# Performance work log

Measured on AMD Instinct MI355X. Metric: run time of the kernel, lower is better.

Reference implementation:

```python
import jax, jax.numpy as jnp
import numpy as np

EPS = 1e-5

def lrelu(x):
    return jnp.where(x > 0, x, 0.2 * x)

def bn(x, g, b, ch_axis=1):
    # BatchNorm in training-mode math (batch statistics), affine
    axes = tuple(i for i in range(x.ndim) if i != ch_axis)
    m = x.mean(axes, keepdims=True)
    v = x.var(axes, keepdims=True)
    shp = [1] * x.ndim; shp[ch_axis] = -1
    return g.reshape(shp) * (x - m) / jnp.sqrt(v + EPS) + b.reshape(shp)

def get_graph_feature(x, idx):
    # x: (B,C,N), idx: (B,N,k) -> edge features (B,2C,N,k) = [neighbor - center, center]
    xt = jnp.transpose(x, (0, 2, 1))                      # (B,N,C)
    nb = jax.vmap(lambda pts, i: pts[i])(xt, idx)         # gather: (B,N,k,C)
    center = jnp.broadcast_to(xt[:, :, None, :], nb.shape)
    edge = jnp.concatenate([nb - center, center], axis=-1)  # (B,N,k,2C)
    return jnp.transpose(edge, (0, 3, 1, 2))              # (B,2C,N,k)

def setup_inputs() -> dict:
    key = jax.random.key(0)
    ks = jax.random.split(key, 12)
    B, N, K = 4, 2048, 20
    def w(k, o, c, s=0.05):
        return jax.random.normal(k, (o, c), jnp.float32) * s
    inp = {}
    inp["x"] = jax.random.normal(ks[0], (B, N, 3), jnp.float32)
    inp["start_neighs"] = jax.random.randint(ks[1], (B, N, K), 0, N)
    dims = [(6, 64), (128, 128), (256, 256), (512, 512)]
    for i, (ci, co) in enumerate(dims):
        inp["w%d" % i] = w(ks[2 + i], co, ci)
        inp["g%d" % i] = jnp.ones((co,), jnp.float32)
        inp["b%d" % i] = jnp.zeros((co,), jnp.float32)
    inp["w4"] = w(ks[6], 1024, 960)
    inp["g4"] = jnp.ones((1024,), jnp.float32); inp["b4"] = jnp.zeros((1024,), jnp.float32)
    inp["lw1"] = w(ks[7], 1024, 2048)
    inp["g6"] = jnp.ones((1024,), jnp.float32); inp["b6"] = jnp.zeros((1024,), jnp.float32)
    inp["lw2"] = w(ks[8], 512, 1024); inp["lb2"] = jnp.zeros((512,), jnp.float32)
    inp["g7"] = jnp.ones((512,), jnp.float32); inp["b7"] = jnp.zeros((512,), jnp.float32)
    inp["lw3"] = w(ks[9], 256, 512); inp["lb3"] = jnp.zeros((256,), jnp.float32)
    return inp

def reference(x, start_neighs,
              w0, g0, b0, w1, g1, b1, w2, g2, b2, w3, g3, b3,
              w4, g4, b4, lw1, g6, b6, lw2, lb2, g7, b7, lw3, lb3):
    # forward_per_point
    xt = jnp.transpose(x, (0, 2, 1))                      # (B,3,N)
    h = get_graph_feature(xt, start_neighs)               # (B,6,N,k)
    outs = []
    for (w, g, b) in ((w0, g0, b0), (w1, g1, b1), (w2, g2, b2), (w3, g3, b3)):
        if outs:  # only_true_neighs=True -> reuse start_neighs
            h = get_graph_feature(outs[-1], start_neighs)
        h = lrelu(bn(jnp.einsum('oc,bcnk->bonk', w, h), g, b))  # 1x1 Conv2d + BN + LeakyReLU
        outs.append(h.max(axis=-1))                       # max over k neighbors -> (B,C,N)
    cat = jnp.concatenate(outs, axis=1)                   # (B,960,N)
    feats = lrelu(bn(jnp.einsum('oc,bcn->bon', w4, cat), g4, b4))  # (B,1024,N)
    # aggregate_all_points (dropout p=0 -> identity)
    z = jnp.concatenate([feats.max(-1), feats.mean(-1)], axis=1)   # (B,2048)
    z = lrelu(bn(z @ lw1.T, g6, b6))
    z = lrelu(bn(z @ lw2.T + lb2, g7, b7))
    z = z @ lw3.T + lb3                                   # (B,256)
    # forward returns (aggregated.squeeze(-1), features_per_point.transpose(1,2)) = (z, (B,1024,N))
    return z, feats
```

## Files before the change

kernel.cpp:

```cpp
#include <hip/hip_runtime.h>
#include <cstddef>
#include <cstdint>

#define EPSBN 1e-5f
constexpr int B_ = 4, N_ = 2048, K_ = 20;

typedef __attribute__((ext_vector_type(8))) _Float16 half8v;
typedef __attribute__((ext_vector_type(4))) float f32x4;
typedef const __attribute__((address_space(1))) unsigned int* gas_t;
typedef __attribute__((address_space(3))) unsigned int* las_t;

__device__ __forceinline__ void swz_batch(int B, int& b, int& local) {
    b = (B & 7) >> 1;
    local = ((B >> 3) << 1) | (B & 1);
}


__device__ __forceinline__ void prep_conv(const float* __restrict__ W, _Float16* __restrict__ W2h,
                                          int O, int C, int i) {
    int o = i / C, c = i - o * C;
    float a = W[o * 2 * C + c];
    float d = W[o * 2 * C + C + c] - a;
    W2h[(size_t)o * C + c] = (_Float16)a;
    W2h[(size_t)(O + o) * C + c] = (_Float16)d;
}

__global__ void k_prep_all(const float* __restrict__ w1, const float* __restrict__ w2,
                           const float* __restrict__ w3, const float* __restrict__ w4,
                           _Float16* __restrict__ W2h1, _Float16* __restrict__ W2h2,
                           _Float16* __restrict__ W2h3, _Float16* __restrict__ w4h) {
    int i = blockIdx.x * 256 + threadIdx.x;
    if (i < 8192) { prep_conv(w1, W2h1, 128, 64, i); return; }
    i -= 8192;
    if (i < 32768) { prep_conv(w2, W2h2, 256, 128, i); return; }
    i -= 32768;
    if (i < 131072) { prep_conv(w3, W2h3, 512, 256, i); return; }
    i -= 131072;
    if (i < 983040) w4h[i] = (_Float16)w4[i];
}

__global__ void k_dense0(const float* __restrict__ x, const float* __restrict__ w0,
                         _Float16* __restrict__ Z0) {
    int b, local;
    swz_batch(blockIdx.x, b, local);
    int i = (b * 1024 + local) * 256 + threadIdx.x;
    int p = i >> 7, o = i & 127;
    float x0 = x[p * 3], x1 = x[p * 3 + 1], x2 = x[p * 3 + 2];
    float r;
    if (o < 64) {
        r = x0 * w0[o * 6] + x1 * w0[o * 6 + 1] + x2 * w0[o * 6 + 2];
    } else {
        int oo = o - 64;
        r = x0 * (w0[oo * 6 + 3] - w0[oo * 6]) + x1 * (w0[oo * 6 + 4] - w0[oo * 6 + 1]) +
            x2 * (w0[oo * 6 + 5] - w0[oo * 6 + 2]);
    }
    Z0[i] = (_Float16)r;
}

template<bool STATS>
__global__ __launch_bounds__(256, 3)
void k_gemm(const _Float16* __restrict__ A, int sa,
            const _Float16* __restrict__ Bw, int K,
            _Float16* __restrict__ outp, int so,
            float* __restrict__ psum, float* __restrict__ psq) {
    __shared__ __align__(16) _Float16 Als[128 * 64];
    __shared__ __align__(16) _Float16 Bls[128 * 64];
    const int tid = threadIdx.x, lane = tid & 63, w = tid >> 6;
    int bsw, lsw;
    swz_batch(blockIdx.x, bsw, lsw);
    const int m0 = (bsw * 16 + lsw) * 128;
    const int n0 = blockIdx.y * 128;
    const int wr = (w >> 1) * 64, wc = (w & 1) * 64;

    f32x4 acc[4][4];
#pragma unroll
    for (int i = 0; i < 4; ++i)
#pragma unroll
        for (int j = 0; j < 4; ++j) acc[i][j] = (f32x4){0.f, 0.f, 0.f, 0.f};

    int srow[4], scol[4];
#pragma unroll
    for (int j = 0; j < 4; ++j) {
        int idx = w * 256 + j * 64 + lane;
        srow[j] = idx >> 3;
        scol[j] = ((idx & 7) ^ (srow[j] & 7)) * 8;
    }
    int aoff[4][2], boff[4][2];
#pragma unroll
    for (int i = 0; i < 4; ++i) {
        int ra = wr + i * 16 + (lane & 15);
        int rb = wc + i * 16 + (lane & 15);
#pragma unroll
        for (int t = 0; t < 2; ++t) {
            aoff[i][t] = ra * 64 + ((((lane >> 4) + t * 4) ^ (ra & 7)) * 8);
            boff[i][t] = rb * 64 + ((((lane >> 4) + t * 4) ^ (rb & 7)) * 8);
        }
    }

    for (int c0 = 0; c0 < K; c0 += 64) {
#pragma unroll
        for (int j = 0; j < 4; ++j) {
            const _Float16* ga = &A[(size_t)(m0 + srow[j]) * sa + c0 + scol[j]];
            const _Float16* gb = &Bw[(size_t)(n0 + srow[j]) * K + c0 + scol[j]];
            __builtin_amdgcn_global_load_lds((gas_t)(const void*)ga,
                                             (las_t)(void*)&Als[(w * 256 + j * 64) * 8], 16, 0, 0);
            __builtin_amdgcn_global_load_lds((gas_t)(const void*)gb,
                                             (las_t)(void*)&Bls[(w * 256 + j * 64) * 8], 16, 0, 0);
        }
        __syncthreads();
#pragma unroll
        for (int t = 0; t < 2; ++t) {
            half8v a[4], b[4];
#pragma unroll
            for (int i = 0; i < 4; ++i) {
                a[i] = *(const half8v*)&Als[aoff[i][t]];
                b[i] = *(const half8v*)&Bls[boff[i][t]];
            }
#pragma unroll
            for (int i = 0; i < 4; ++i)
#pragma unroll
                for (int j = 0; j < 4; ++j)
                    acc[i][j] = __builtin_amdgcn_mfma_f32_16x16x32_f16(a[i], b[j], acc[i][j], 0, 0, 0);
        }
        __syncthreads();
    }
#pragma unroll
    for (int i = 0; i < 4; ++i)
#pragma unroll
        for (int j = 0; j < 4; ++j)
#pragma unroll
            for (int e = 0; e < 4; ++e) {
                int row = m0 + wr + i * 16 + (lane >> 4) * 4 + e;
                int col = n0 + wc + j * 16 + (lane & 15);
                outp[(size_t)row * so + col] = (_Float16)acc[i][j][e];
            }
    if constexpr (STATS) {
        int slice = blockIdx.x & 63;
#pragma unroll
        for (int j = 0; j < 4; ++j) {
            float s = 0.f, q = 0.f;
#pragma unroll
            for (int i = 0; i < 4; ++i)
#pragma unroll
                for (int e = 0; e < 4; ++e) {
                    float v = acc[i][j][e];
                    s += v; q += v * v;
                }
            s += __shfl_xor(s, 16); s += __shfl_xor(s, 32);
            q += __shfl_xor(q, 16); q += __shfl_xor(q, 32);
            if ((lane >> 4) == 0) {
                int col = n0 + wc + j * 16 + lane;
                atomicAdd(&psum[slice * 1024 + col], s);
                atomicAdd(&psq[slice * 1024 + col], q);
            }
        }
    }
}

template<int O>
__global__ __launch_bounds__(256)
void k_gather(const _Float16* __restrict__ Z, const int* __restrict__ nidx,
              const float* __restrict__ g,
              _Float16* __restrict__ exth,
              float* __restrict__ psum, float* __restrict__ psq) {
    constexpr int VPT = O / 8, P = 256 / VPT;
    __shared__ float s_red[P * O];
    __shared__ float q_red[P * O];
    const int tid = threadIdx.x;
    const int pl = tid / VPT, v = tid % VPT;
    int bsw, local;
    swz_batch(blockIdx.x, bsw, local);
    const int bbase = bsw * N_;
    const int p = bbase + local * P + pl;
    float sg[8];
#pragma unroll
    for (int e = 0; e < 8; ++e) sg[e] = (g[v * 8 + e] >= 0.f) ? 1.f : -1.f;
    float mx[8], sm[8], sq[8];
#pragma unroll
    for (int e = 0; e < 8; ++e) { mx[e] = -3.4e38f; sm[e] = 0.f; sq[e] = 0.f; }
    const int* np = nidx + p * K_;
#pragma unroll 4
    for (int k = 0; k < K_; ++k) {
        int j = np[k];
        half8v z = *(const half8v*)&Z[(size_t)(bbase + j) * (2 * O) + v * 8];
#pragma unroll
        for (int e = 0; e < 8; ++e) {
            float f = (float)z[e];
            mx[e] = fmaxf(mx[e], f * sg[e]);
            sm[e] += f;
            sq[e] += f * f;
        }
    }
    half8v zd = *(const half8v*)&Z[(size_t)p * (2 * O) + O + v * 8];
    const float Kf = (float)K_;
    half8v exo;
#pragma unroll
    for (int e = 0; e < 8; ++e) {
        float zf = (float)zd[e];
        exo[e] = (_Float16)(sg[e] * mx[e] + zf);
        s_red[pl * O + v * 8 + e] = sm[e] + Kf * zf;
        q_red[pl * O + v * 8 + e] = sq[e] + 2.f * zf * sm[e] + Kf * zf * zf;
    }
    *(half8v*)&exth[(size_t)p * O + v * 8] = exo;
    __syncthreads();
    int slice = blockIdx.x & 63;
    for (int ch = tid; ch < O; ch += 256) {
        float s = 0.f, q = 0.f;
#pragma unroll
        for (int pp = 0; pp < P; ++pp) { s += s_red[pp * O + ch]; q += q_red[pp * O + ch]; }
        atomicAdd(&psum[slice * 1024 + ch], s);
        atomicAdd(&psq[slice * 1024 + ch], q);
    }
}

__global__ void k_finalize_sl(const float* __restrict__ psum, const float* __restrict__ psq,
                              const float* __restrict__ g, const float* __restrict__ b,
                              float cntInv, int O,
                              float* __restrict__ scale, float* __restrict__ shift) {
    int o = blockIdx.x * 256 + threadIdx.x;
    if (o >= O) return;
    float s = 0.f, q = 0.f;
    for (int i = 0; i < 64; ++i) { s += psum[i * 1024 + o]; q += psq[i * 1024 + o]; }
    float m = s * cntInv;
    float v = q * cntInv - m * m;
    float sc = g[o] * rsqrtf(fmaxf(v, 0.f) + EPSBN);
    scale[o] = sc;
    shift[o] = b[o] - m * sc;
}

template<int O>
__global__ void k_bn_apply(const _Float16* __restrict__ exth,
                           const float* __restrict__ scale, const float* __restrict__ shift,
                           _Float16* __restrict__ cath, int coff) {
    constexpr int PPB = 2048 / O;
    int bsw, local;
    swz_batch(blockIdx.x, bsw, local);
    const int pt_base = bsw * N_ + local * PPB;
    int tid = threadIdx.x;
    int pt = pt_base + (tid * 8) / O;
    int v8 = (tid * 8) & (O - 1);
    half8v hx = *(const half8v*)&exth[(size_t)pt * O + v8];
    half8v r;
#pragma unroll
    for (int e = 0; e < 8; ++e) {
        int o = v8 + e;
        float y = scale[o] * (float)hx[e] + shift[o];
        y = y > 0.f ? y : 0.2f * y;
        r[e] = (_Float16)y;
    }
    *(half8v*)&cath[(size_t)pt * 960 + coff + v8] = r;
}

__global__ void k_feats_out(const _Float16* __restrict__ Y4, const float* __restrict__ scale,
                            const float* __restrict__ shift, float* __restrict__ fo,
                            float* __restrict__ pmax, float* __restrict__ psumn) {
    __shared__ float tile[32][33];
    int tx = threadIdx.x, ty = threadIdx.y;
    int b = blockIdx.z;
    int n0 = blockIdx.x * 32, c0 = blockIdx.y * 32;
#pragma unroll
    for (int i = 0; i < 4; ++i) {
        int n = n0 + ty + i * 8;
        int c = c0 + tx;
        float v = (float)Y4[((size_t)(b * N_ + n)) * 1024 + c];
        v = scale[c] * v + shift[c];
        v = v > 0.f ? v : 0.2f * v;
        tile[ty + i * 8][tx] = v;
    }
    __syncthreads();
#pragma unroll
    for (int i = 0; i < 4; ++i) {
        int c = c0 + ty + i * 8;
        int n = n0 + tx;
        float v2 = tile[tx][ty + i * 8];
        fo[((size_t)(b * 1024 + c)) * N_ + n] = v2;
        float mx = v2, s = v2;
#pragma unroll
        for (int d = 1; d < 32; d <<= 1) {
            mx = fmaxf(mx, __shfl_xor(mx, d));
            s += __shfl_xor(s, d);
        }
        if (tx == 0) {
            int bc = (b << 10) + c;
            pmax[(size_t)bc * 64 + blockIdx.x] = mx;
            psumn[(size_t)bc * 64 + blockIdx.x] = s;
        }
    }
}

__global__ void k_pool2(const float* __restrict__ pmax, const float* __restrict__ psumn,
                        float* __restrict__ z0) {
    int bc = blockIdx.x * 4 + (threadIdx.x >> 6);
    int lane = threadIdx.x & 63;
    float mx = pmax[(size_t)bc * 64 + lane];
    float s  = psumn[(size_t)bc * 64 + lane];
#pragma unroll
    for (int d = 1; d < 64; d <<= 1) {
        mx = fmaxf(mx, __shfl_xor(mx, d));
        s += __shfl_xor(s, d);
    }
    if (lane == 0) {
        int b = bc >> 10, c = bc & 1023;
        z0[b * 2048 + c] = mx;
        z0[b * 2048 + 1024 + c] = s * (1.f / N_);
    }
}

__global__ void k_fc(const float* __restrict__ zin, const float* __restrict__ W,
                     const float* __restrict__ bias,
                     const float* __restrict__ gg, const float* __restrict__ gb,
                     int C, int O, float* __restrict__ zout) {
    __shared__ float sh4[4];
    const int b = threadIdx.x >> 6;
    const int lane = threadIdx.x & 63;
    const int o = blockIdx.x;
    const float* wr = W + (size_t)o * C;
    const float* zr = zin + b * C;
    float s = 0.f;
    for (int c = lane * 4; c < C; c += 256) {
        const float4 wv = *(const float4*)&wr[c];
        const float4 zv = *(const float4*)&zr[c];
        s += wv.x * zv.x + wv.y * zv.y + wv.z * zv.z + wv.w * zv.w;
    }
    s += __shfl_xor(s, 1);
    s += __shfl_xor(s, 2);
    s += __shfl_xor(s, 4);
    s += __shfl_xor(s, 8);
    s += __shfl_xor(s, 16);
    s += __shfl_xor(s, 32);
    if (!gg) {
        if (lane == 0) zout[b * O + o] = s + (bias ? bias[o] : 0.f);
        return;
    }
    if (lane == 0) sh4[b] = s + (bias ? bias[o] : 0.f);
    __syncthreads();
    if (threadIdx.x == 0) {
        float v0 = sh4[0], v1 = sh4[1], v2 = sh4[2], v3 = sh4[3];
        float m = 0.25f * (v0 + v1 + v2 + v3);
        float d0 = v0 - m, d1 = v1 - m, d2 = v2 - m, d3 = v3 - m;
        float var = 0.25f * (d0 * d0 + d1 * d1 + d2 * d2 + d3 * d3);
        float sc = gg[o] * rsqrtf(var + EPSBN);
        float shv = gb[o];
        float r0 = sc * d0 + shv, r1 = sc * d1 + shv, r2 = sc * d2 + shv, r3 = sc * d3 + shv;
        zout[o]         = r0 > 0.f ? r0 : 0.2f * r0;
        zout[O + o]     = r1 > 0.f ? r1 : 0.2f * r1;
        zout[2 * O + o] = r2 > 0.f ? r2 : 0.2f * r2;
        zout[3 * O + o] = r3 > 0.f ? r3 : 0.2f * r3;
    }
}


extern "C" void kernel_launch(void* const* d_in, const int* in_sizes, int n_in,
                              void* d_out, int out_size, void* d_ws, size_t ws_size,
                              hipStream_t stream) {
    const float* x    = (const float*)d_in[0];
    const int*   nidx = (const int*)d_in[1];
    const float* w[5]  = {(const float*)d_in[2], (const float*)d_in[5], (const float*)d_in[8],
                          (const float*)d_in[11], (const float*)d_in[14]};
    const float* g[5]  = {(const float*)d_in[3], (const float*)d_in[6], (const float*)d_in[9],
                          (const float*)d_in[12], (const float*)d_in[15]};
    const float* bb[5] = {(const float*)d_in[4], (const float*)d_in[7], (const float*)d_in[10],
                          (const float*)d_in[13], (const float*)d_in[16]};
    const float* lw1 = (const float*)d_in[17];
    const float* g6  = (const float*)d_in[18];
    const float* b6  = (const float*)d_in[19];
    const float* lw2 = (const float*)d_in[20];
    const float* lb2 = (const float*)d_in[21];
    const float* g7  = (const float*)d_in[22];
    const float* b7  = (const float*)d_in[23];
    const float* lw3 = (const float*)d_in[24];
    const float* lb3 = (const float*)d_in[25];

    float* out = (float*)d_out;
    float* fo  = out + 1024;

    uint8_t* base8 = (uint8_t*)d_ws;
    size_t off = 0;
    auto alloc = [&](size_t bytes) -> void* {
        void* r = base8 + off;
        off += (bytes + 255) & ~(size_t)255;
        return r;
    };
    _Float16* cath = (_Float16*)alloc((size_t)B_ * N_ * 960 * 2);
    _Float16* Z    = (_Float16*)alloc((size_t)8192 * 1024 * 2);
    _Float16* exth = (_Float16*)alloc((size_t)8192 * 512 * 2);
    _Float16* Y4   = (_Float16*)alloc((size_t)8192 * 1024 * 2);
    _Float16* W2h1 = (_Float16*)alloc((size_t)256 * 64 * 2);
    _Float16* W2h2 = (_Float16*)alloc((size_t)512 * 128 * 2);
    _Float16* W2h3 = (_Float16*)alloc((size_t)1024 * 256 * 2);
    _Float16* w4h  = (_Float16*)alloc((size_t)1024 * 960 * 2);
    float* psumall = (float*)alloc((size_t)5 * 131072 * 4);
    float* pmax  = (float*)alloc((size_t)4096 * 64 * 4);
    float* psumn = (float*)alloc((size_t)4096 * 64 * 4);
    float* scalev= (float*)alloc(1024 * 4);
    float* shiftv= (float*)alloc(1024 * 4);
    float* z0    = (float*)alloc(8192 * 4);
    float* z1    = (float*)alloc(4096 * 4);
    float* z2    = (float*)alloc(2048 * 4);
    (void)ws_size; (void)in_sizes; (void)n_in; (void)out_size;

    auto psumR = [&](int r) { return psumall + (size_t)r * 131072; };
    auto psqR  = [&](int r) { return psumall + (size_t)r * 131072 + 65536; };

    hipMemsetAsync(psumall, 0, (size_t)5 * 131072 * 4, stream);
    k_prep_all<<<(8192 + 32768 + 131072 + 983040 + 255) / 256, 256, 0, stream>>>(
        w[1], w[2], w[3], w[4], W2h1, W2h2, W2h3, w4h);

    k_dense0<<<4096, 256, 0, stream>>>(x, w[0], Z);
    k_gather<64><<<256, 256, 0, stream>>>(Z, nidx, g[0], exth, psumR(0), psqR(0));
    k_finalize_sl<<<1, 256, 0, stream>>>(psumR(0), psqR(0), g[0], bb[0], 1.f / (B_ * N_ * K_),
                                         64, scalev, shiftv);
    k_bn_apply<64><<<256, 256, 0, stream>>>(exth, scalev, shiftv, cath, 0);

    struct LayerCfg { int coff_in, C, O, coff_out, li; const _Float16* Wh; };
    const LayerCfg L[3] = {
        { 0,   64,  128, 64,  1, W2h1 },
        { 64,  128, 256, 192, 2, W2h2 },
        { 192, 256, 512, 448, 3, W2h3 },
    };
    for (int i = 0; i < 3; ++i) {
        const LayerCfg& Lc = L[i];
        dim3 ggrid(64, (2 * Lc.O) / 128);
        k_gemm<false><<<ggrid, 256, 0, stream>>>(cath + Lc.coff_in, 960, Lc.Wh, Lc.C,
                                                 Z, 2 * Lc.O, nullptr, nullptr);
        if (Lc.O == 128) {
            k_gather<128><<<512, 256, 0, stream>>>(Z, nidx, g[Lc.li], exth, psumR(i + 1), psqR(i + 1));
            k_finalize_sl<<<1, 256, 0, stream>>>(psumR(i + 1), psqR(i + 1), g[Lc.li], bb[Lc.li],
                                                 1.f / (B_ * N_ * K_), 128, scalev, shiftv);
            k_bn_apply<128><<<512, 256, 0, stream>>>(exth, scalev, shiftv, cath, Lc.coff_out);
        } else if (Lc.O == 256) {
            k_gather<256><<<1024, 256, 0, stream>>>(Z, nidx, g[Lc.li], exth, psumR(i + 1), psqR(i + 1));
            k_finalize_sl<<<1, 256, 0, stream>>>(psumR(i + 1), psqR(i + 1), g[Lc.li], bb[Lc.li],
                                                 1.f / (B_ * N_ * K_), 256, scalev, shiftv);
            k_bn_apply<256><<<1024, 256, 0, stream>>>(exth, scalev, shiftv, cath, Lc.coff_out);
        } else {
            k_gather<512><<<2048, 256, 0, stream>>>(Z, nidx, g[Lc.li], exth, psumR(i + 1), psqR(i + 1));
            k_finalize_sl<<<2, 256, 0, stream>>>(psumR(i + 1), psqR(i + 1), g[Lc.li], bb[Lc.li],
                                                 1.f / (B_ * N_ * K_), 512, scalev, shiftv);
            k_bn_apply<512><<<2048, 256, 0, stream>>>(exth, scalev, shiftv, cath, Lc.coff_out);
        }
    }

    k_gemm<true><<<dim3(64, 8), 256, 0, stream>>>(cath, 960, w4h, 960, Y4, 1024, psumR(4), psqR(4));
    k_finalize_sl<<<4, 256, 0, stream>>>(psumR(4), psqR(4), g[4], bb[4], 1.f / (B_ * N_), 1024,
                                         scalev, shiftv);
    k_feats_out<<<dim3(64, 32, 4), dim3(32, 8), 0, stream>>>(Y4, scalev, shiftv, fo, pmax, psumn);
    k_pool2<<<1024, 256, 0, stream>>>(pmax, psumn, z0);

    k_fc<<<1024, 256, 0, stream>>>(z0, lw1, nullptr, g6, b6, 2048, 1024, z1);
    k_fc<<<512, 256, 0, stream>>>(z1, lw2, lb2, g7, b7, 1024, 512, z2);
    k_fc<<<256, 256, 0, stream>>>(z2, lw3, lb3, nullptr, nullptr, 512, 256, out);
}
```

Measured before the change: 172.0 us.

## Fuse BN stat finalization into producers via last-block counter; fuse layer-0 dense into gather

Removes the separate k_finalize_sl launches by having the last block of each stats-producing kernel (tracked with an atomic counter and threadfence) compute the BN scale and shift. It also folds the layer-0 pointwise conv into a new gather kernel that computes features directly from xyz coordinates, which drops k_dense0 and its Z round-trip. Together these remove five launches and one intermediate buffer write. The cost is a serialized tail in one block per kernel, plus extra atomic counter traffic.

Result: slower. 552.8 us (+221.3%).

```diff
diff --git a/kernel.cpp b/kernel.cpp
--- a/kernel.cpp
+++ b/kernel.cpp
@@ -13,6 +13,39 @@
 __device__ __forceinline__ void swz_batch(int B, int& b, int& local) {
     b = (B & 7) >> 1;
     local = ((B >> 3) << 1) | (B & 1);
+}
+
+__device__ __forceinline__ float agent_load(const float* p) {
+    return __hip_atomic_load(p, __ATOMIC_RELAXED, __HIP_MEMORY_SCOPE_AGENT);
+}
+
+__device__ __forceinline__ void finalize_tail(const float* __restrict__ psum,
+                                              const float* __restrict__ psq,
+                                              const float* __restrict__ g,
+                                              const float* __restrict__ b,
+                                              float cntInv, int O, int nblk,
+                                              float* __restrict__ scale,
+                                              float* __restrict__ shift,
+                                              int* __restrict__ cnt) {
+    __shared__ int s_last;
+    __threadfence();
+    __syncthreads();
+    if (threadIdx.x == 0) s_last = (atomicAdd(cnt, 1) == nblk - 1);
+    __syncthreads();
+    if (!s_last) return;
+    for (int o = threadIdx.x; o < O; o += 256) {
+        float s = 0.f, q = 0.f;
+#pragma unroll 8
+        for (int i = 0; i < 64; ++i) {
+            s += agent_load(&psum[i * 1024 + o]);
+            q += agent_load(&psq[i * 1024 + o]);
+        }
+        float m = s * cntInv;
+        float v = q * cntInv - m * m;
+        float sc = g[o] * rsqrtf(fmaxf(v, 0.f) + EPSBN);
+        scale[o] = sc;
+        shift[o] = b[o] - m * sc;
+    }
 }
 
 
@@ -39,30 +72,14 @@
     if (i < 983040) w4h[i] = (_Float16)w4[i];
 }
 
-__global__ void k_dense0(const float* __restrict__ x, const float* __restrict__ w0,
-                         _Float16* __restrict__ Z0) {
-    int b, local;
-    swz_batch(blockIdx.x, b, local);
-    int i = (b * 1024 + local) * 256 + threadIdx.x;
-    int p = i >> 7, o = i & 127;
-    float x0 = x[p * 3], x1 = x[p * 3 + 1], x2 = x[p * 3 + 2];
-    float r;
-    if (o < 64) {
-        r = x0 * w0[o * 6] + x1 * w0[o * 6 + 1] + x2 * w0[o * 6 + 2];
-    } else {
-        int oo = o - 64;
-        r = x0 * (w0[oo * 6 + 3] - w0[oo * 6]) + x1 * (w0[oo * 6 + 4] - w0[oo * 6 + 1]) +
-            x2 * (w0[oo * 6 + 5] - w0[oo * 6 + 2]);
-    }
-    Z0[i] = (_Float16)r;
-}
-
 template<bool STATS>
 __global__ __launch_bounds__(256, 3)
 void k_gemm(const _Float16* __restrict__ A, int sa,
             const _Float16* __restrict__ Bw, int K,
             _Float16* __restrict__ outp, int so,
-            float* __restrict__ psum, float* __restrict__ psq) {
+            float* __restrict__ psum, float* __restrict__ psq,
+            const float* __restrict__ gvec, const float* __restrict__ bvec,
+            float* __restrict__ scale, float* __restrict__ shift, int* __restrict__ cnt) {
     __shared__ __align__(16) _Float16 Als[128 * 64];
     __shared__ __align__(16) _Float16 Bls[128 * 64];
     const int tid = threadIdx.x, lane = tid & 63, w = tid >> 6;
@@ -154,15 +171,85 @@
                 atomicAdd(&psq[slice * 1024 + col], q);
             }
         }
-    }
+        finalize_tail(psum, psq, gvec, bvec, 1.f / (B_ * N_), 1024,
+                      (int)(gridDim.x * gridDim.y), scale, shift, cnt);
+    }
+}
+
+__global__ __launch_bounds__(256)
+void k_gather0(const float* __restrict__ x, const float* __restrict__ w0,
+               const int* __restrict__ nidx, const float* __restrict__ g,
+               const float* __restrict__ bvec,
+               _Float16* __restrict__ exth,
+               float* __restrict__ psum, float* __restrict__ psq,
+               float* __restrict__ scale, float* __restrict__ shift, int* __restrict__ cnt) {
+    constexpr int O = 64, VPT = 8, P = 32;
+    __shared__ float s_red[P * O];
+    __shared__ float q_red[P * O];
+    const int tid = threadIdx.x;
+    const int pl = tid / VPT, v = tid % VPT;
+    int bsw, local;
+    swz_batch(blockIdx.x, bsw, local);
+    const int bbase = bsw * N_;
+    const int p = bbase + local * P + pl;
+    float wa[8][3], wd[8][3], sg[8];
+#pragma unroll
+    for (int e = 0; e < 8; ++e) {
+        int o = v * 8 + e;
+        float a0 = w0[o * 6], a1 = w0[o * 6 + 1], a2 = w0[o * 6 + 2];
+        wa[e][0] = a0; wa[e][1] = a1; wa[e][2] = a2;
+        wd[e][0] = w0[o * 6 + 3] - a0;
+        wd[e][1] = w0[o * 6 + 4] - a1;
+        wd[e][2] = w0[o * 6 + 5] - a2;
+        sg[e] = (g[o] >= 0.f) ? 1.f : -1.f;
+    }
+    float mx[8], sm[8], sq[8];
+#pragma unroll
+    for (int e = 0; e < 8; ++e) { mx[e] = -3.4e38f; sm[e] = 0.f; sq[e] = 0.f; }
+    const int* np = nidx + p * K_;
+#pragma unroll 4
+    for (int k = 0; k < K_; ++k) {
+        int j = bbase + np[k];
+        float x0 = x[j * 3], x1 = x[j * 3 + 1], x2 = x[j * 3 + 2];
+#pragma unroll
+        for (int e = 0; e < 8; ++e) {
+            float f = wa[e][0] * x0 + wa[e][1] * x1 + wa[e][2] * x2;
+            mx[e] = fmaxf(mx[e], f * sg[e]);
+            sm[e] += f;
+            sq[e] += f * f;
+        }
+    }
+    float xp0 = x[p * 3], xp1 = x[p * 3 + 1], xp2 = x[p * 3 + 2];
+    const float Kf = (float)K_;
+    half8v exo;
+#pragma unroll
+    for (int e = 0; e < 8; ++e) {
+        float zf = wd[e][0] * xp0 + wd[e][1] * xp1 + wd[e][2] * xp2;
+        exo[e] = (_Float16)(sg[e] * mx[e] + zf);
+        s_red[pl * O + v * 8 + e] = sm[e] + Kf * zf;
+        q_red[pl * O + v * 8 + e] = sq[e] + 2.f * zf * sm[e] + Kf * zf * zf;
+    }
+    *(half8v*)&exth[(size_t)p * O + v * 8] = exo;
+    __syncthreads();
+    int slice = blockIdx.x & 63;
+    for (int ch = tid; ch < O; ch += 256) {
+        float s = 0.f, q = 0.f;
+#pragma unroll
+        for (int pp = 0; pp < P; ++pp) { s += s_red[pp * O + ch]; q += q_red[pp * O + ch]; }
+        atomicAdd(&psum[slice * 1024 + ch], s);
+        atomicAdd(&psq[slice * 1024 + ch], q);
+    }
+    finalize_tail(psum, psq, g, bvec, 1.f / (B_ * N_ * K_), O, (int)gridDim.x,
+                  scale, shift, cnt);
 }
 
 template<int O>
 __global__ __launch_bounds__(256)
 void k_gather(const _Float16* __restrict__ Z, const int* __restrict__ nidx,
-              const float* __restrict__ g,
+              const float* __restrict__ g, const float* __restrict__ bvec,
               _Float16* __restrict__ exth,
-              float* __restrict__ psum, float* __restrict__ psq) {
+              float* __restrict__ psum, float* __restrict__ psq,
+              float* __restrict__ scale, float* __restrict__ shift, int* __restrict__ cnt) {
     constexpr int VPT = O / 8, P = 256 / VPT;
     __shared__ float s_red[P * O];
     __shared__ float q_red[P * O];
@@ -211,21 +298,8 @@
         atomicAdd(&psum[slice * 1024 + ch], s);
         atomicAdd(&psq[slice * 1024 + ch], q);
     }
-}
-
-__global__ void k_finalize_sl(const float* __restrict__ psum, const float* __restrict__ psq,
-                              const float* __restrict__ g, const float* __restrict__ b,
-                              float cntInv, int O,
-                              float* __restrict__ scale, float* __restrict__ shift) {
-    int o = blockIdx.x * 256 + threadIdx.x;
-    if (o >= O) return;
-    float s = 0.f, q = 0.f;
-    for (int i = 0; i < 64; ++i) { s += psum[i * 1024 + o]; q += psq[i * 1024 + o]; }
-    float m = s * cntInv;
-    float v = q * cntInv - m * m;
-    float sc = g[o] * rsqrtf(fmaxf(v, 0.f) + EPSBN);
-    scale[o] = sc;
-    shift[o] = b[o] - m * sc;
+    finalize_tail(psum, psq, g, bvec, 1.f / (B_ * N_ * K_), O, (int)gridDim.x,
+                  scale, shift, cnt);
 }
 
 template<int O>
@@ -390,6 +464,7 @@
     _Float16* W2h3 = (_Float16*)alloc((size_t)1024 * 256 * 2);
     _Float16* w4h  = (_Float16*)alloc((size_t)1024 * 960 * 2);
     float* psumall = (float*)alloc((size_t)5 * 131072 * 4);
+    int*   cnts    = (int*)alloc(256);
     float* pmax  = (float*)alloc((size_t)4096 * 64 * 4);
     float* psumn = (float*)alloc((size_t)4096 * 64 * 4);
     float* scalev= (float*)alloc(1024 * 4);
@@ -402,14 +477,12 @@
     auto psumR = [&](int r) { return psumall + (size_t)r * 131072; };
     auto psqR  = [&](int r) { return psumall + (size_t)r * 131072 + 65536; };
 
-    hipMemsetAsync(psumall, 0, (size_t)5 * 131072 * 4, stream);
+    hipMemsetAsync(psumall, 0, (size_t)5 * 131072 * 4 + 256, stream);
     k_prep_all<<<(8192 + 32768 + 131072 + 983040 + 255) / 256, 256, 0, stream>>>(
         w[1], w[2], w[3], w[4], W2h1, W2h2, W2h3, w4h);
 
-    k_dense0<<<4096, 256, 0, stream>>>(x, w[0], Z);
-    k_gather<64><<<256, 256, 0, stream>>>(Z, nidx, g[0], exth, psumR(0), psqR(0));
-    k_finalize_sl<<<1, 256, 0, stream>>>(psumR(0), psqR(0), g[0], bb[0], 1.f / (B_ * N_ * K_),
-                                         64, scalev, shiftv);
+    k_gather0<<<256, 256, 0, stream>>>(x, w[0], nidx, g[0], bb[0], exth,
+                                       psumR(0), psqR(0), scalev, shiftv, cnts + 0);
     k_bn_apply<64><<<256, 256, 0, stream>>>(exth, scalev, shiftv, cath, 0);
 
     struct LayerCfg { int coff_in, C, O, coff_out, li; const _Float16* Wh; };
@@ -422,28 +495,29 @@
         const LayerCfg& Lc = L[i];
         dim3 ggrid(64, (2 * Lc.O) / 128);
         k_gemm<false><<<ggrid, 256, 0, stream>>>(cath + Lc.coff_in, 960, Lc.Wh, Lc.C,
-                                                 Z, 2 * Lc.O, nullptr, nullptr);
+                                                 Z, 2 * Lc.O, nullptr, nullptr,
+                                                 nullptr, nullptr, nullptr, nullptr, nullptr);
         if (Lc.O == 128) {
-            k_gather<128><<<512, 256, 0, stream>>>(Z, nidx, g[Lc.li], exth, psumR(i + 1), psqR(i + 1));
-            k_finalize_sl<<<1, 256, 0, stream>>>(psumR(i + 1), psqR(i + 1), g[Lc.li], bb[Lc.li],
-                                                 1.f / (B_ * N_ * K_), 128, scalev, shiftv);
+            k_gather<128><<<512, 256, 0, stream>>>(Z, nidx, g[Lc.li], bb[Lc.li], exth,
+                                                   psumR(i + 1), psqR(i + 1),
+                                                   scalev, shiftv, cnts + i + 1);
             k_bn_apply<128><<<512, 256, 0, stream>>>(exth, scalev, shiftv, cath, Lc.coff_out);
         } else if (Lc.O == 256) {
-            k_gather<256><<<1024, 256, 0, stream>>>(Z, nidx, g[Lc.li], exth, psumR(i + 1), psqR(i + 1));
-            k_finalize_sl<<<1, 256, 0, stream>>>(psumR(i + 1), psqR(i + 1), g[Lc.li], bb[Lc.li],
-                                                 1.f / (B_ * N_ * K_), 256, scalev, shiftv);
+            k_gather<256><<<1024, 256, 0, stream>>>(Z, nidx, g[Lc.li], bb[Lc.li], exth,
+                                                    psumR(i + 1), psqR(i + 1),
+                                                    scalev, shiftv, cnts + i + 1);
             k_bn_apply<256><<<1024, 256, 0, stream>>>(exth, scalev, shiftv, cath, Lc.coff_out);
         } else {
-            k_gather<512><<<2048, 256, 0, stream>>>(Z, nidx, g[Lc.li], exth, psumR(i + 1), psqR(i + 1));
-            k_finalize_sl<<<2, 256, 0, stream>>>(psumR(i + 1), psqR(i + 1), g[Lc.li], bb[Lc.li],
-                                                 1.f / (B_ * N_ * K_), 512, scalev, shiftv);
+            k_gather<512><<<2048, 256, 0, stream>>>(Z, nidx, g[Lc.li], bb[Lc.li], exth,
+                                                    psumR(i + 1), psqR(i + 1),
+                                                    scalev, shiftv, cnts + i + 1);
             k_bn_apply<512><<<2048, 256, 0, stream>>>(exth, scalev, shiftv, cath, Lc.coff_out);
         }
     }
 
-    k_gemm<true><<<dim3(64, 8), 256, 0, stream>>>(cath, 960, w4h, 960, Y4, 1024, psumR(4), psqR(4));
-    k_finalize_sl<<<4, 256, 0, stream>>>(psumR(4), psqR(4), g[4], bb[4], 1.f / (B_ * N_), 1024,
-                                         scalev, shiftv);
+    k_gemm<true><<<dim3(64, 8), 256, 0, stream>>>(cath, 960, w4h, 960, Y4, 1024,
+                                                  psumR(4), psqR(4), g[4], bb[4],
+                                                  scalev, shiftv, cnts + 4);
     k_feats_out<<<dim3(64, 32, 4), dim3(32, 8), 0, stream>>>(Y4, scalev, shiftv, fo, pmax, psumn);
     k_pool2<<<1024, 256, 0, stream>>>(pmax, psumn, z0);
 
```
